# Optimization experiments

Hardware: AMD Instinct MI355X
Metric: run time of the kernel (lower is better)

## Reference

```python
import jax, jax.numpy as jnp
import numpy as np

B, M, N, T = 8192, 4, 8, 512  # groups, measurements, states, timesteps


def setup_inputs() -> dict:
    key = jax.random.key(0)
    k0, k1, k2, k3, k4, k5 = jax.random.split(key, 6)
    x = jax.random.normal(k0, (B, M, T), dtype=jnp.float32)
    # stable transition matrix (spectral radius < 1)
    F = (0.9 * jnp.eye(N) + 0.05 * jax.random.normal(k1, (N, N)) / np.sqrt(N)).astype(jnp.float32)
    H = (jax.random.normal(k2, (M, N)) / np.sqrt(N)).astype(jnp.float32)
    qa = jax.random.normal(k3, (N, N))
    Q = (0.05 * (qa @ qa.T) / N + 0.01 * jnp.eye(N)).astype(jnp.float32)
    ra = jax.random.normal(k4, (M, M))
    R = (0.1 * (ra @ ra.T) / M + 0.05 * jnp.eye(M)).astype(jnp.float32)
    initial_std_dev = (1.0 + jax.random.uniform(k5, (N,))).astype(jnp.float32)
    return {"x": x, "F": F, "H": H, "Q": Q, "R": R, "initial_std_dev": initial_std_dev}


def _kf_forward(x, F, H, Q, R, initial_std_dev):
    b, m, t = x.shape
    n = F.shape[0]
    dt = x.dtype
    # default_initializer: mean = 0 (len(initial_state)==num_states path with zeros),
    # cov = quad_form_diag(std, eye) = diag(std^2)
    mean0 = jnp.zeros((b, n, 1), dt)
    cov0 = jnp.broadcast_to(jnp.diag(initial_std_dev ** 2).astype(dt), (b, n, n))
    I_n = jnp.eye(n, dtype=dt)

    def step(carry, obs_t):  # obs_t: [b, m]
        mu, P = carry  # [b,n,1], [b,n,n]
        # --- predict ---
        mu = jnp.einsum('ij,bjk->bik', F, mu)
        P = jnp.einsum('ij,bjk,lk->bil', F, P, F) + Q
        out = jnp.einsum('mj,bjo->bmo', H, mu)[..., 0]  # [b, m]
        # --- update (no NaNs in obs -> update all slices) ---
        resid = obs_t[..., None] - out[..., None]  # [b,m,1]
        HP = jnp.einsum('mj,bjk->bmk', H, P)  # [b,m,n]
        S = jnp.einsum('bmj,nj->bmn', HP, H) + R  # [b,m,m]
        Sinv = jnp.linalg.inv(S)
        PHt = jnp.swapaxes(HP, 1, 2)  # P symmetric => P H^T = (H P)^T, [b,n,m]
        K = jnp.einsum('bnm,bmo->bno', PHt, Sinv)  # [b,n,m]
        mu_new = mu + jnp.einsum('bnm,bmo->bno', K, resid)
        # Joseph-stabilized covariance update
        ImKH = I_n - jnp.einsum('bnm,mj->bnj', K, H)  # [b,n,n]
        P_new = (jnp.einsum('bij,bjk,blk->bil', ImKH, P, ImKH)
                 + jnp.einsum('bim,mo,bko->bik', K, R, K))
        return (mu_new, P_new), out

    xs = jnp.moveaxis(x, 2, 0)  # [t, b, m]
    _, outs = jax.lax.scan(step, (mean0, cov0), xs)
    return jnp.moveaxis(outs, 0, 2)  # [b, m, t]


def reference(x, F, H, Q, R, initial_std_dev):
    return _kf_forward(x, F, H, Q, R, initial_std_dev)
```

## Files before the change

### kernel.cpp

```cpp
#include <hip/hip_runtime.h>


#define B_BATCH 8192
#define M_MEAS 4
#define N_ST 8
#define T_STEPS 512
#define CHUNK 16
#define NCHUNK (T_STEPS / CHUNK)

__device__ __forceinline__ void kf_producer(
    const float* __restrict__ Fp, const float* __restrict__ Hp,
    const float* __restrict__ Qp, const float* __restrict__ Rp,
    const float* __restrict__ stdp, float* __restrict__ Kws, int* flag)
{
    const int lane = threadIdx.x;
    const int i = lane >> 3, j = lane & 7;
    __shared__ float Pm[64], T1m[64], Um[32], PPm[64], Km[32], Am[64], Hs[32];

    float Fi[8], Fj[8], Hm[4][8], HFm[4][8], HFr[8], QHi[4];
    float R2[4][4], Rr[4][4];
#pragma unroll
    for (int k = 0; k < 8; ++k) { Fi[k] = Fp[8 * i + k]; Fj[k] = Fp[8 * j + k]; }
#pragma unroll
    for (int m = 0; m < 4; ++m)
#pragma unroll
        for (int k = 0; k < 8; ++k) Hm[m][k] = Hp[8 * m + k];
#pragma unroll
    for (int m = 0; m < 4; ++m)
#pragma unroll
        for (int c = 0; c < 8; ++c) {
            float a = 0.f;
#pragma unroll
            for (int k = 0; k < 8; ++k) a += Hm[m][k] * Fp[8 * k + c];
            HFm[m][c] = a;
        }
#pragma unroll
    for (int c = 0; c < 8; ++c) {
        float a = 0.f;
#pragma unroll
        for (int k = 0; k < 8; ++k) a += Hp[8 * (i & 3) + k] * Fp[8 * k + c];
        HFr[c] = a;
    }
    const float Qij = Qp[lane];
#pragma unroll
    for (int m = 0; m < 4; ++m) {
        float a = 0.f;
#pragma unroll
        for (int k = 0; k < 8; ++k) a += Qp[8 * i + k] * Hm[m][k];
        QHi[m] = a;
    }
    {
        float HQ[4][8];
#pragma unroll
        for (int m = 0; m < 4; ++m)
#pragma unroll
            for (int c = 0; c < 8; ++c) {
                float a = 0.f;
#pragma unroll
                for (int l = 0; l < 8; ++l) a += Hm[m][l] * Qp[8 * l + c];
                HQ[m][c] = a;
            }
#pragma unroll
        for (int m = 0; m < 4; ++m)
#pragma unroll
            for (int n = 0; n < 4; ++n) {
                float a = Rp[4 * m + n];
#pragma unroll
                for (int k = 0; k < 8; ++k) a += HQ[m][k] * Hm[n][k];
                R2[m][n] = a;
                Rr[m][n] = Rp[4 * m + n];
            }
    }
    if (i < 4) Hs[8 * i + j] = Hp[8 * i + j];
    float pold;
    { float s0 = stdp[i]; pold = (i == j) ? s0 * s0 : 0.f; Pm[lane] = pold; }
    __syncthreads();

    int convcnt = 0;
    for (int t = 0; t < T_STEPS; ++t) {
        float Pc[8];
#pragma unroll
        for (int k = 0; k < 8; ++k) Pc[k] = Pm[8 * k + j];
        float t1 = 0.f, uo = 0.f;
#pragma unroll
        for (int k = 0; k < 8; ++k) { t1 += Fi[k] * Pc[k]; uo += HFr[k] * Pc[k]; }
        T1m[lane] = t1;
        if (i < 4) Um[8 * i + j] = uo;
        __syncthreads();

        float T1r[8];
#pragma unroll
        for (int k = 0; k < 8; ++k) T1r[k] = T1m[8 * i + k];
        float pp = Qij;
#pragma unroll
        for (int k = 0; k < 8; ++k) pp += T1r[k] * Fj[k];
        float PPH[4];
#pragma unroll
        for (int m = 0; m < 4; ++m) {
            float a = QHi[m];
#pragma unroll
            for (int k = 0; k < 8; ++k) a += T1r[k] * HFm[m][k];
            PPH[m] = a;
        }
        PPm[lane] = pp;

        float Ur[4][8];
#pragma unroll
        for (int m = 0; m < 4; ++m)
#pragma unroll
            for (int k = 0; k < 8; ++k) Ur[m][k] = Um[8 * m + k];
        float S[4][4];
#pragma unroll
        for (int m = 0; m < 4; ++m)
#pragma unroll
            for (int n = m; n < 4; ++n) {
                float a = R2[m][n];
#pragma unroll
                for (int k = 0; k < 8; ++k) a += Ur[m][k] * HFm[n][k];
                S[m][n] = a; S[n][m] = a;
            }
        float SI[16];
        {
            const float A0 = S[0][0], A1 = S[0][1], A2 = S[0][2], A3 = S[0][3];
            const float A4 = S[1][0], A5 = S[1][1], A6 = S[1][2], A7 = S[1][3];
            const float A8 = S[2][0], A9 = S[2][1], A10 = S[2][2], A11 = S[2][3];
            const float A12 = S[3][0], A13 = S[3][1], A14 = S[3][2], A15 = S[3][3];
            float b00 = A0 * A5 - A1 * A4, b01 = A0 * A6 - A2 * A4;
            float b02 = A0 * A7 - A3 * A4, b03 = A1 * A6 - A2 * A5;
            float b04 = A1 * A7 - A3 * A5, b05 = A2 * A7 - A3 * A6;
            float b06 = A8 * A13 - A9 * A12, b07 = A8 * A14 - A10 * A12;
            float b08 = A8 * A15 - A11 * A12, b09 = A9 * A14 - A10 * A13;
            float b10 = A9 * A15 - A11 * A13, b11 = A10 * A15 - A11 * A14;
            float det = b00 * b11 - b01 * b10 + b02 * b09 + b03 * b08 -
                        b04 * b07 + b05 * b06;
            float rd = 1.0f / det;
            SI[0]  = ( A5 * b11 - A6 * b10 + A7 * b09) * rd;
            SI[1]  = (-A1 * b11 + A2 * b10 - A3 * b09) * rd;
            SI[2]  = ( A13 * b05 - A14 * b04 + A15 * b03) * rd;
            SI[3]  = (-A9 * b05 + A10 * b04 - A11 * b03) * rd;
            SI[4]  = (-A4 * b11 + A6 * b08 - A7 * b07) * rd;
            SI[5]  = ( A0 * b11 - A2 * b08 + A3 * b07) * rd;
            SI[6]  = (-A12 * b05 + A14 * b02 - A15 * b01) * rd;
            SI[7]  = ( A8 * b05 - A10 * b02 + A11 * b01) * rd;
            SI[8]  = ( A4 * b10 - A5 * b08 + A7 * b06) * rd;
            SI[9]  = (-A0 * b10 + A1 * b08 - A3 * b06) * rd;
            SI[10] = ( A12 * b04 - A13 * b02 + A15 * b00) * rd;
            SI[11] = (-A8 * b04 + A9 * b02 - A11 * b00) * rd;
            SI[12] = (-A4 * b09 + A5 * b07 - A6 * b06) * rd;
            SI[13] = ( A0 * b09 - A1 * b07 + A2 * b06) * rd;
            SI[14] = (-A12 * b03 + A13 * b01 - A14 * b00) * rd;
            SI[15] = ( A8 * b03 - A9 * b01 + A10 * b00) * rd;
        }
        float Kl[4];
#pragma unroll
        for (int m = 0; m < 4; ++m) {
            float a = 0.f;
#pragma unroll
            for (int p = 0; p < 4; ++p) a += PPH[p] * SI[4 * p + m];
            Kl[m] = a;
        }
        if (j < 4) {
            const float kj = (j == 0) ? Kl[0] : (j == 1) ? Kl[1]
                           : (j == 2) ? Kl[2] : Kl[3];
            Km[4 * i + j] = kj;
            Kws[t * 32 + i * 4 + j] = kj;
        }
        float Ar[8];
#pragma unroll
        for (int c = 0; c < 8; ++c) {
            float a = (i == c) ? 1.f : 0.f;
#pragma unroll
            for (int m = 0; m < 4; ++m) a -= Kl[m] * Hm[m][c];
            Ar[c] = a;
        }
        {
            float aij = (i == j) ? 1.f : 0.f;
#pragma unroll
            for (int m = 0; m < 4; ++m) aij -= Kl[m] * Hs[8 * m + j];
            Am[lane] = aij;
        }
        float Ei[4];
#pragma unroll
        for (int o = 0; o < 4; ++o) {
            float a = 0.f;
#pragma unroll
            for (int m = 0; m < 4; ++m) a += Kl[m] * Rr[m][o];
            Ei[o] = a;
        }
        __syncthreads();

        float Arj[8], Kj[4];
#pragma unroll
        for (int k = 0; k < 8; ++k) Arj[k] = Am[8 * j + k];
#pragma unroll
        for (int o = 0; o < 4; ++o) Kj[o] = Km[4 * j + o];
        float acc = 0.f;
#pragma unroll
        for (int l = 0; l < 8; ++l) {
            float rdot = 0.f;
#pragma unroll
            for (int k = 0; k < 8; ++k) rdot += PPm[8 * l + k] * Arj[k];
            acc += Ar[l] * rdot;
        }
#pragma unroll
        for (int o = 0; o < 4; ++o) acc += Ei[o] * Kj[o];
        Pm[lane] = acc;

        const float dp = fabsf(acc - pold);
        pold = acc;
        convcnt = __all(dp <= 4e-7f) ? convcnt + 1 : 0;
        if (convcnt >= 2 && t >= 47 && t < T_STEPS - 1) {
            if (j < 4) {
                const float kj = (j == 0) ? Kl[0] : (j == 1) ? Kl[1]
                               : (j == 2) ? Kl[2] : Kl[3];
                for (int tt = t + 1; tt < T_STEPS; ++tt)
                    Kws[tt * 32 + i * 4 + j] = kj;
            }
            if (flag != nullptr && lane == 0) {
                __hip_atomic_store(flag + 1, t, __ATOMIC_RELAXED,
                                   __HIP_MEMORY_SCOPE_AGENT);
                __threadfence();
                __hip_atomic_store(flag, NCHUNK, __ATOMIC_RELEASE,
                                   __HIP_MEMORY_SCOPE_AGENT);
            }
            break;
        }

        if (flag != nullptr && ((t & (CHUNK - 1)) == (CHUNK - 1))) {
            if (lane == 0) {
                __threadfence();
                __hip_atomic_store(flag, (t + 1) / CHUNK, __ATOMIC_RELEASE,
                                   __HIP_MEMORY_SCOPE_AGENT);
            }
        }
        __syncthreads();
    }
}

__device__ __forceinline__ void kf_consumer(
    const float* __restrict__ xp, const float* __restrict__ Fp,
    const float* __restrict__ Hp, const float* __restrict__ Kws,
    float* __restrict__ outp, int bblk, int* flag)
{
    const int b = bblk * 64 + threadIdx.x;

    float Fv[N_ST][N_ST];
#pragma unroll
    for (int n = 0; n < N_ST; ++n)
#pragma unroll
        for (int k = 0; k < N_ST; ++k) Fv[n][k] = Fp[8 * n + k];

    float G[M_MEAS][N_ST];
#pragma unroll
    for (int m = 0; m < M_MEAS; ++m) {
#pragma unroll
        for (int n = 0; n < N_ST; ++n) {
            float acc = 0.f;
#pragma unroll
            for (int k = 0; k < N_ST; ++k) acc += Hp[8 * m + k] * Fv[k][n];
            G[m][n] = acc;
        }
    }

    float mu[N_ST];
#pragma unroll
    for (int n = 0; n < N_ST; ++n) mu[n] = 0.f;

    const float* xb = xp + (size_t)b * (M_MEAS * T_STEPS);
    float* ob = outp + (size_t)b * (M_MEAS * T_STEPS);

    float4 xq[M_MEAS];
#pragma unroll
    for (int m = 0; m < M_MEAS; ++m)
        xq[m] = *(const float4*)(xb + m * T_STEPS);

    int lastseen = 0, tcf = 0;
    int t4 = 0;
    for (; t4 < T_STEPS / 4; ++t4) {
        if (flag != nullptr && (t4 & 3) == 0) {
            const int need = (t4 >> 2) + 1;
            if (lastseen < need) {
                while ((lastseen = __hip_atomic_load(
                            flag, __ATOMIC_RELAXED,
                            __HIP_MEMORY_SCOPE_AGENT)) < need)
                    __builtin_amdgcn_s_sleep(16);
                __builtin_amdgcn_fence(__ATOMIC_ACQUIRE, "agent");
            }
            if (tcf == 0)
                tcf = __hip_atomic_load(flag + 1, __ATOMIC_RELAXED,
                                        __HIP_MEMORY_SCOPE_AGENT);
            if (tcf > 0 && t4 * 4 >= tcf) break;
        }

        float4 xn[M_MEAS] = {xq[0], xq[1], xq[2], xq[3]};
        if (t4 + 1 < T_STEPS / 4) {
#pragma unroll
            for (int m = 0; m < M_MEAS; ++m)
                xn[m] = *(const float4*)(xb + m * T_STEPS + (t4 + 1) * 4);
        }

        float obuf[M_MEAS][4];
#pragma unroll
        for (int s = 0; s < 4; ++s) {
            const int t = t4 * 4 + s;
            const float4* kq = (const float4*)(Kws + t * 32);
            float4 kv[N_ST];
#pragma unroll
            for (int n = 0; n < N_ST; ++n) kv[n] = kq[n];

            float resid[M_MEAS];
#pragma unroll
            for (int m = 0; m < M_MEAS; ++m) {
                float acc = 0.f;
#pragma unroll
                for (int n = 0; n < N_ST; ++n) acc += G[m][n] * mu[n];
                obuf[m][s] = acc;
                const float xv = (s == 0) ? xq[m].x
                               : (s == 1) ? xq[m].y
                               : (s == 2) ? xq[m].z : xq[m].w;
                resid[m] = xv - acc;
            }
            float nmu[N_ST];
#pragma unroll
            for (int n = 0; n < N_ST; ++n) {
                float acc = 0.f;
#pragma unroll
                for (int k = 0; k < N_ST; ++k) acc += Fv[n][k] * mu[k];
                acc += kv[n].x * resid[0] + kv[n].y * resid[1] +
                       kv[n].z * resid[2] + kv[n].w * resid[3];
                nmu[n] = acc;
            }
#pragma unroll
            for (int n = 0; n < N_ST; ++n) mu[n] = nmu[n];
        }

#pragma unroll
        for (int m = 0; m < M_MEAS; ++m) {
            *(float4*)(ob + m * T_STEPS + t4 * 4) =
                make_float4(obuf[m][0], obuf[m][1], obuf[m][2], obuf[m][3]);
        }
#pragma unroll
        for (int m = 0; m < M_MEAS; ++m) xq[m] = xn[m];
    }

    if (t4 < T_STEPS / 4) {
        float4 kvF[N_ST];
        {
            const float4* kqF = (const float4*)(Kws + (t4 * 4) * 32);
#pragma unroll
            for (int n = 0; n < N_ST; ++n) kvF[n] = kqF[n];
        }
        for (; t4 < T_STEPS / 4; ++t4) {
            float4 xn[M_MEAS] = {xq[0], xq[1], xq[2], xq[3]};
            if (t4 + 1 < T_STEPS / 4) {
#pragma unroll
                for (int m = 0; m < M_MEAS; ++m)
                    xn[m] = *(const float4*)(xb + m * T_STEPS + (t4 + 1) * 4);
            }

            float obuf[M_MEAS][4];
#pragma unroll
            for (int s = 0; s < 4; ++s) {
                float resid[M_MEAS];
#pragma unroll
                for (int m = 0; m < M_MEAS; ++m) {
                    float acc = 0.f;
#pragma unroll
                    for (int n = 0; n < N_ST; ++n) acc += G[m][n] * mu[n];
                    obuf[m][s] = acc;
                    const float xv = (s == 0) ? xq[m].x
                                   : (s == 1) ? xq[m].y
                                   : (s == 2) ? xq[m].z : xq[m].w;
                    resid[m] = xv - acc;
                }
                float nmu[N_ST];
#pragma unroll
                for (int n = 0; n < N_ST; ++n) {
                    float acc = 0.f;
#pragma unroll
                    for (int k = 0; k < N_ST; ++k) acc += Fv[n][k] * mu[k];
                    acc += kvF[n].x * resid[0] + kvF[n].y * resid[1] +
                           kvF[n].z * resid[2] + kvF[n].w * resid[3];
                    nmu[n] = acc;
                }
#pragma unroll
                for (int n = 0; n < N_ST; ++n) mu[n] = nmu[n];
            }

#pragma unroll
            for (int m = 0; m < M_MEAS; ++m) {
                *(float4*)(ob + m * T_STEPS + t4 * 4) =
                    make_float4(obuf[m][0], obuf[m][1], obuf[m][2], obuf[m][3]);
            }
#pragma unroll
            for (int m = 0; m < M_MEAS; ++m) xq[m] = xn[m];
        }
    }
}

__global__ __launch_bounds__(64) void kf_kernel(
    const float* __restrict__ x, const float* __restrict__ F,
    const float* __restrict__ H, const float* __restrict__ Q,
    const float* __restrict__ R, const float* __restrict__ std0,
    float* __restrict__ Kws, int* flag, float* __restrict__ out, int role)
{
    if (role == 0) {
        if (blockIdx.x == 0) kf_producer(F, H, Q, R, std0, Kws, flag);
        else kf_consumer(x, F, H, Kws, out, (int)blockIdx.x - 1, flag);
    } else if (role == 1) {
        kf_producer(F, H, Q, R, std0, Kws, nullptr);
    } else {
        kf_consumer(x, F, H, Kws, out, (int)blockIdx.x, nullptr);
    }
}

extern "C" void kernel_launch(void* const* d_in, const int* in_sizes, int n_in,
                              void* d_out, int out_size, void* d_ws, size_t ws_size,
                              hipStream_t stream) {
    const float* x   = (const float*)d_in[0];
    const float* F   = (const float*)d_in[1];
    const float* H   = (const float*)d_in[2];
    const float* Q   = (const float*)d_in[3];
    const float* R   = (const float*)d_in[4];
    const float* s0  = (const float*)d_in[5];
    float* out = (float*)d_out;
    float* Kws = (float*)d_ws;
    const size_t KWS_BYTES = (size_t)T_STEPS * 32 * sizeof(float);

    if (ws_size >= KWS_BYTES + 256) {
        int* flag = (int*)((char*)d_ws + KWS_BYTES);
        hipMemsetAsync(flag, 0, 2 * sizeof(int), stream);
        kf_kernel<<<dim3(1 + B_BATCH / 64), dim3(64), 0, stream>>>(
            x, F, H, Q, R, s0, Kws, flag, out, 0);
    } else {
        kf_kernel<<<dim3(1), dim3(64), 0, stream>>>(
            x, F, H, Q, R, s0, Kws, (int*)nullptr, out, 1);
        kf_kernel<<<dim3(B_BATCH / 64), dim3(64), 0, stream>>>(
            x, F, H, Q, R, s0, Kws, (int*)nullptr, out, 2);
    }
}
```

Baseline: 409.1 us.

## Restructure Kalman producer covariance update and batch consumer by 16-step chunks

The producer's Joseph covariance update changes from an O(n^3)-per-thread triple product to two stages of dot products through shared memory, with an extra barrier. Shared-memory reads become float4 vector loads, and the redundant H copy in shared memory is dropped. The consumer now processes 16 timesteps per flag check and stores outputs in 16-element groups. The steady-state gain detection threshold is loosened (1.5e-6, earliest step 31 instead of 47), so the producer stops sooner and the consumer switches to a fixed gain earlier, at some cost in accuracy.

```diff
diff --git a/kernel.cpp b/kernel.cpp
--- a/kernel.cpp
+++ b/kernel.cpp
@@ -15,7 +15,7 @@
 {
     const int lane = threadIdx.x;
     const int i = lane >> 3, j = lane & 7;
-    __shared__ float Pm[64], T1m[64], Um[32], PPm[64], Km[32], Am[64], Hs[32];
+    __shared__ float Pm[64], T1m[64], Vm[32], PPm[64], Am[64], Bm[64], Km[32];
 
     float Fi[8], Fj[8], Hm[4][8], HFm[4][8], HFr[8], QHi[4];
     float R2[4][4], Rr[4][4];
@@ -71,26 +71,25 @@
                 Rr[m][n] = Rp[4 * m + n];
             }
     }
-    if (i < 4) Hs[8 * i + j] = Hp[8 * i + j];
     float pold;
     { float s0 = stdp[i]; pold = (i == j) ? s0 * s0 : 0.f; Pm[lane] = pold; }
     __syncthreads();
 
     int convcnt = 0;
     for (int t = 0; t < T_STEPS; ++t) {
-        float Pc[8];
-#pragma unroll
-        for (int k = 0; k < 8; ++k) Pc[k] = Pm[8 * k + j];
+        float4 pa = *(const float4*)&Pm[8 * j];
+        float4 pb = *(const float4*)&Pm[8 * j + 4];
+        float Pc[8] = {pa.x, pa.y, pa.z, pa.w, pb.x, pb.y, pb.z, pb.w};
         float t1 = 0.f, uo = 0.f;
 #pragma unroll
         for (int k = 0; k < 8; ++k) { t1 += Fi[k] * Pc[k]; uo += HFr[k] * Pc[k]; }
         T1m[lane] = t1;
-        if (i < 4) Um[8 * i + j] = uo;
+        if (i < 4) Vm[8 * i + j] = uo;
         __syncthreads();
 
-        float T1r[8];
-#pragma unroll
-        for (int k = 0; k < 8; ++k) T1r[k] = T1m[8 * i + k];
+        float4 ta = *(const float4*)&T1m[8 * i];
+        float4 tb = *(const float4*)&T1m[8 * i + 4];
+        float T1r[8] = {ta.x, ta.y, ta.z, ta.w, tb.x, tb.y, tb.z, tb.w};
         float pp = Qij;
 #pragma unroll
         for (int k = 0; k < 8; ++k) pp += T1r[k] * Fj[k];
@@ -104,11 +103,14 @@
         }
         PPm[lane] = pp;
 
-        float Ur[4][8];
-#pragma unroll
-        for (int m = 0; m < 4; ++m)
-#pragma unroll
-            for (int k = 0; k < 8; ++k) Ur[m][k] = Um[8 * m + k];
+        float Vr[4][8];
+#pragma unroll
+        for (int m = 0; m < 4; ++m) {
+            float4 va = *(const float4*)&Vm[8 * m];
+            float4 vb = *(const float4*)&Vm[8 * m + 4];
+            Vr[m][0] = va.x; Vr[m][1] = va.y; Vr[m][2] = va.z; Vr[m][3] = va.w;
+            Vr[m][4] = vb.x; Vr[m][5] = vb.y; Vr[m][6] = vb.z; Vr[m][7] = vb.w;
+        }
         float S[4][4];
 #pragma unroll
         for (int m = 0; m < 4; ++m)
@@ -116,7 +118,7 @@
             for (int n = m; n < 4; ++n) {
                 float a = R2[m][n];
 #pragma unroll
-                for (int k = 0; k < 8; ++k) a += Ur[m][k] * HFm[n][k];
+                for (int k = 0; k < 8; ++k) a += Vr[m][k] * HFm[n][k];
                 S[m][n] = a; S[n][m] = a;
             }
         float SI[16];
@@ -159,12 +161,6 @@
             for (int p = 0; p < 4; ++p) a += PPH[p] * SI[4 * p + m];
             Kl[m] = a;
         }
-        if (j < 4) {
-            const float kj = (j == 0) ? Kl[0] : (j == 1) ? Kl[1]
-                           : (j == 2) ? Kl[2] : Kl[3];
-            Km[4 * i + j] = kj;
-            Kws[t * 32 + i * 4 + j] = kj;
-        }
         float Ar[8];
 #pragma unroll
         for (int c = 0; c < 8; ++c) {
@@ -173,12 +169,6 @@
             for (int m = 0; m < 4; ++m) a -= Kl[m] * Hm[m][c];
             Ar[c] = a;
         }
-        {
-            float aij = (i == j) ? 1.f : 0.f;
-#pragma unroll
-            for (int m = 0; m < 4; ++m) aij -= Kl[m] * Hs[8 * m + j];
-            Am[lane] = aij;
-        }
         float Ei[4];
 #pragma unroll
         for (int o = 0; o < 4; ++o) {
@@ -187,34 +177,50 @@
             for (int m = 0; m < 4; ++m) a += Kl[m] * Rr[m][o];
             Ei[o] = a;
         }
+        const float aij = (j == 0) ? Ar[0] : (j == 1) ? Ar[1]
+                        : (j == 2) ? Ar[2] : (j == 3) ? Ar[3]
+                        : (j == 4) ? Ar[4] : (j == 5) ? Ar[5]
+                        : (j == 6) ? Ar[6] : Ar[7];
+        Am[lane] = aij;
+        const float kj4 = (j == 0) ? Kl[0] : (j == 1) ? Kl[1]
+                        : (j == 2) ? Kl[2] : Kl[3];
+        if (j < 4) {
+            Km[4 * i + j] = kj4;
+            Kws[t * 32 + i * 4 + j] = kj4;
+        }
         __syncthreads();
 
-        float Arj[8], Kj[4];
-#pragma unroll
-        for (int k = 0; k < 8; ++k) Arj[k] = Am[8 * j + k];
-#pragma unroll
-        for (int o = 0; o < 4; ++o) Kj[o] = Km[4 * j + o];
+        float4 qa = *(const float4*)&PPm[8 * j];
+        float4 qb = *(const float4*)&PPm[8 * j + 4];
+        float PPc[8] = {qa.x, qa.y, qa.z, qa.w, qb.x, qb.y, qb.z, qb.w};
+        float bv = 0.f;
+#pragma unroll
+        for (int k = 0; k < 8; ++k) bv += Ar[k] * PPc[k];
+        Bm[lane] = bv;
+        float4 aja = *(const float4*)&Am[8 * j];
+        float4 ajb = *(const float4*)&Am[8 * j + 4];
+        float Arj[8] = {aja.x, aja.y, aja.z, aja.w, ajb.x, ajb.y, ajb.z, ajb.w};
+        float4 kjv = *(const float4*)&Km[4 * j];
+        float Kj[4] = {kjv.x, kjv.y, kjv.z, kjv.w};
+        __syncthreads();
+
+        float4 ba = *(const float4*)&Bm[8 * i];
+        float4 bb = *(const float4*)&Bm[8 * i + 4];
+        float Br[8] = {ba.x, ba.y, ba.z, ba.w, bb.x, bb.y, bb.z, bb.w};
         float acc = 0.f;
 #pragma unroll
-        for (int l = 0; l < 8; ++l) {
-            float rdot = 0.f;
-#pragma unroll
-            for (int k = 0; k < 8; ++k) rdot += PPm[8 * l + k] * Arj[k];
-            acc += Ar[l] * rdot;
-        }
+        for (int k = 0; k < 8; ++k) acc += Br[k] * Arj[k];
 #pragma unroll
         for (int o = 0; o < 4; ++o) acc += Ei[o] * Kj[o];
         Pm[lane] = acc;
 
         const float dp = fabsf(acc - pold);
         pold = acc;
-        convcnt = __all(dp <= 4e-7f) ? convcnt + 1 : 0;
-        if (convcnt >= 2 && t >= 47 && t < T_STEPS - 1) {
+        convcnt = __all(dp <= 1.5e-6f) ? convcnt + 1 : 0;
+        if (convcnt >= 2 && t >= 31 && t < T_STEPS - 1) {
             if (j < 4) {
-                const float kj = (j == 0) ? Kl[0] : (j == 1) ? Kl[1]
-                               : (j == 2) ? Kl[2] : Kl[3];
                 for (int tt = t + 1; tt < T_STEPS; ++tt)
-                    Kws[tt * 32 + i * 4 + j] = kj;
+                    Kws[tt * 32 + i * 4 + j] = kj4;
             }
             if (flag != nullptr && lane == 0) {
                 __hip_atomic_store(flag + 1, t, __ATOMIC_RELAXED,
@@ -269,16 +275,11 @@
     const float* xb = xp + (size_t)b * (M_MEAS * T_STEPS);
     float* ob = outp + (size_t)b * (M_MEAS * T_STEPS);
 
-    float4 xq[M_MEAS];
-#pragma unroll
-    for (int m = 0; m < M_MEAS; ++m)
-        xq[m] = *(const float4*)(xb + m * T_STEPS);
-
     int lastseen = 0, tcf = 0;
-    int t4 = 0;
-    for (; t4 < T_STEPS / 4; ++t4) {
-        if (flag != nullptr && (t4 & 3) == 0) {
-            const int need = (t4 >> 2) + 1;
+    int g = 0;
+    for (; g < 32; ++g) {
+        if (flag != nullptr) {
+            const int need = g + 1;
             if (lastseen < need) {
                 while ((lastseen = __hip_atomic_load(
                             flag, __ATOMIC_RELAXED,
@@ -289,85 +290,33 @@
             if (tcf == 0)
                 tcf = __hip_atomic_load(flag + 1, __ATOMIC_RELAXED,
                                         __HIP_MEMORY_SCOPE_AGENT);
-            if (tcf > 0 && t4 * 4 >= tcf) break;
-        }
-
-        float4 xn[M_MEAS] = {xq[0], xq[1], xq[2], xq[3]};
-        if (t4 + 1 < T_STEPS / 4) {
+            if (tcf > 0 && g * 16 >= tcf) break;
+        }
+
+        float ob16[M_MEAS][16];
+#pragma unroll
+        for (int u = 0; u < 4; ++u) {
+            const int t4 = g * 4 + u;
+            float4 xq[M_MEAS];
 #pragma unroll
             for (int m = 0; m < M_MEAS; ++m)
-                xn[m] = *(const float4*)(xb + m * T_STEPS + (t4 + 1) * 4);
-        }
-
-        float obuf[M_MEAS][4];
-#pragma unroll
-        for (int s = 0; s < 4; ++s) {
-            const int t = t4 * 4 + s;
-            const float4* kq = (const float4*)(Kws + t * 32);
-            float4 kv[N_ST];
-#pragma unroll
-            for (int n = 0; n < N_ST; ++n) kv[n] = kq[n];
-
-            float resid[M_MEAS];
-#pragma unroll
-            for (int m = 0; m < M_MEAS; ++m) {
-                float acc = 0.f;
-#pragma unroll
-                for (int n = 0; n < N_ST; ++n) acc += G[m][n] * mu[n];
-                obuf[m][s] = acc;
-                const float xv = (s == 0) ? xq[m].x
-                               : (s == 1) ? xq[m].y
-                               : (s == 2) ? xq[m].z : xq[m].w;
-                resid[m] = xv - acc;
-            }
-            float nmu[N_ST];
-#pragma unroll
-            for (int n = 0; n < N_ST; ++n) {
-                float acc = 0.f;
-#pragma unroll
-                for (int k = 0; k < N_ST; ++k) acc += Fv[n][k] * mu[k];
-                acc += kv[n].x * resid[0] + kv[n].y * resid[1] +
-                       kv[n].z * resid[2] + kv[n].w * resid[3];
-                nmu[n] = acc;
-            }
-#pragma unroll
-            for (int n = 0; n < N_ST; ++n) mu[n] = nmu[n];
-        }
-
-#pragma unroll
-        for (int m = 0; m < M_MEAS; ++m) {
-            *(float4*)(ob + m * T_STEPS + t4 * 4) =
-                make_float4(obuf[m][0], obuf[m][1], obuf[m][2], obuf[m][3]);
-        }
-#pragma unroll
-        for (int m = 0; m < M_MEAS; ++m) xq[m] = xn[m];
-    }
-
-    if (t4 < T_STEPS / 4) {
-        float4 kvF[N_ST];
-        {
-            const float4* kqF = (const float4*)(Kws + (t4 * 4) * 32);
-#pragma unroll
-            for (int n = 0; n < N_ST; ++n) kvF[n] = kqF[n];
-        }
-        for (; t4 < T_STEPS / 4; ++t4) {
-            float4 xn[M_MEAS] = {xq[0], xq[1], xq[2], xq[3]};
-            if (t4 + 1 < T_STEPS / 4) {
-#pragma unroll
-                for (int m = 0; m < M_MEAS; ++m)
-                    xn[m] = *(const float4*)(xb + m * T_STEPS + (t4 + 1) * 4);
-            }
-
-            float obuf[M_MEAS][4];
+                xq[m] = *(const float4*)(xb + m * T_STEPS + t4 * 4);
+
 #pragma unroll
             for (int s = 0; s < 4; ++s) {
+                const int t = t4 * 4 + s;
+                const float4* kq = (const float4*)(Kws + t * 32);
+                float4 kv[N_ST];
+#pragma unroll
+                for (int n = 0; n < N_ST; ++n) kv[n] = kq[n];
+
                 float resid[M_MEAS];
 #pragma unroll
                 for (int m = 0; m < M_MEAS; ++m) {
                     float acc = 0.f;
 #pragma unroll
                     for (int n = 0; n < N_ST; ++n) acc += G[m][n] * mu[n];
-                    obuf[m][s] = acc;
+                    ob16[m][u * 4 + s] = acc;
                     const float xv = (s == 0) ? xq[m].x
                                    : (s == 1) ? xq[m].y
                                    : (s == 2) ? xq[m].z : xq[m].w;
@@ -379,21 +328,75 @@
                     float acc = 0.f;
 #pragma unroll
                     for (int k = 0; k < N_ST; ++k) acc += Fv[n][k] * mu[k];
-                    acc += kvF[n].x * resid[0] + kvF[n].y * resid[1] +
-                           kvF[n].z * resid[2] + kvF[n].w * resid[3];
+                    acc += kv[n].x * resid[0] + kv[n].y * resid[1] +
+                           kv[n].z * resid[2] + kv[n].w * resid[3];
                     nmu[n] = acc;
                 }
 #pragma unroll
                 for (int n = 0; n < N_ST; ++n) mu[n] = nmu[n];
             }
-
-#pragma unroll
-            for (int m = 0; m < M_MEAS; ++m) {
-                *(float4*)(ob + m * T_STEPS + t4 * 4) =
-                    make_float4(obuf[m][0], obuf[m][1], obuf[m][2], obuf[m][3]);
-            }
-#pragma unroll
-            for (int m = 0; m < M_MEAS; ++m) xq[m] = xn[m];
+        }
+#pragma unroll
+        for (int m = 0; m < M_MEAS; ++m)
+#pragma unroll
+            for (int q = 0; q < 4; ++q)
+                *(float4*)(ob + m * T_STEPS + g * 16 + q * 4) =
+                    make_float4(ob16[m][4 * q], ob16[m][4 * q + 1],
+                                ob16[m][4 * q + 2], ob16[m][4 * q + 3]);
+    }
+
+    if (g < 32) {
+        float4 kvF[N_ST];
+        {
+            const float4* kqF = (const float4*)(Kws + (size_t)(g * 16) * 32);
+#pragma unroll
+            for (int n = 0; n < N_ST; ++n) kvF[n] = kqF[n];
+        }
+        for (; g < 32; ++g) {
+            float ob16[M_MEAS][16];
+#pragma unroll
+            for (int u = 0; u < 4; ++u) {
+                const int t4 = g * 4 + u;
+                float4 xq[M_MEAS];
+#pragma unroll
+                for (int m = 0; m < M_MEAS; ++m)
+                    xq[m] = *(const float4*)(xb + m * T_STEPS + t4 * 4);
+
+#pragma unroll
+                for (int s = 0; s < 4; ++s) {
+                    float resid[M_MEAS];
+#pragma unroll
+                    for (int m = 0; m < M_MEAS; ++m) {
+                        float acc = 0.f;
+#pragma unroll
+                        for (int n = 0; n < N_ST; ++n) acc += G[m][n] * mu[n];
+                        ob16[m][u * 4 + s] = acc;
+                        const float xv = (s == 0) ? xq[m].x
+                                       : (s == 1) ? xq[m].y
+                                       : (s == 2) ? xq[m].z : xq[m].w;
+                        resid[m] = xv - acc;
+                    }
+                    float nmu[N_ST];
+#pragma unroll
+                    for (int n = 0; n < N_ST; ++n) {
+                        float acc = 0.f;
+#pragma unroll
+                        for (int k = 0; k < N_ST; ++k) acc += Fv[n][k] * mu[k];
+                        acc += kvF[n].x * resid[0] + kvF[n].y * resid[1] +
+                               kvF[n].z * resid[2] + kvF[n].w * resid[3];
+                        nmu[n] = acc;
+                    }
+#pragma unroll
+                    for (int n = 0; n < N_ST; ++n) mu[n] = nmu[n];
+                }
+            }
+#pragma unroll
+            for (int m = 0; m < M_MEAS; ++m)
+#pragma unroll
+                for (int q = 0; q < 4; ++q)
+                    *(float4*)(ob + m * T_STEPS + g * 16 + q * 4) =
+                        make_float4(ob16[m][4 * q], ob16[m][4 * q + 1],
+                                    ob16[m][4 * q + 2], ob16[m][4 * q + 3]);
         }
     }
 }
```

New measurement: 355.9 us. 13.0% less time.
